# Performance work log

Measured on AMD Instinct MI355X. Metric: run time of the kernel, lower is better.

The kernel has to match this reference:

```python
import jax, jax.numpy as jnp
import numpy as np

TOP_K = 2  # config.moe_config.top_k


def setup_inputs() -> dict:
    key = jax.random.key(0)
    k0, k1, k2, k3 = jax.random.split(key, 4)
    T, H, I, E = 8192, 2048, 1408, 8  # tokens, hidden, moe_intermediate, experts
    x = jax.random.normal(k0, (T, H), jnp.float32)
    router_weight = jax.random.normal(k1, (E, H), jnp.float32) * 0.02
    gate_up_proj = jax.random.normal(k2, (E, H, 2 * I), jnp.float32) * 0.02
    down_proj = jax.random.normal(k3, (E, I, H), jnp.float32) * 0.02
    return {"x": x, "router_weight": router_weight,
            "gate_up_proj": gate_up_proj, "down_proj": down_proj}


def _moe_forward(x, router_weight, gate_up_proj, down_proj):
    # Router: fp32 gating linear (no bias), softmax over experts, top-k,
    # then scatter the top-k softmax weights into a dense [T, E] gate tensor
    # (topk_version=False path of Router.top_k_softmax).
    T = x.shape[0]
    E = router_weight.shape[0]
    logits = x.astype(jnp.float32) @ router_weight.T            # [T, E]
    probs = jax.nn.softmax(logits, axis=-1)                      # [T, E]
    topk_w, topk_idx = jax.lax.top_k(probs, TOP_K)               # [T, k]
    gates = jnp.zeros_like(logits).at[
        jnp.arange(T)[:, None], topk_idx].set(topk_w)            # [T, E] sparse gates

    # Grouped expert MLP (GroupedMLP): merged gate/up GEMM, SwiGLU, down GEMM.
    # Dispatch/permute + grouped GEMM + weighted combine is mathematically
    # out[t] = sum_e gates[t, e] * MLP_e(x[t]); expressed here as a fixed loop
    # over the small expert set with masked accumulation (jit-friendly).
    out = jnp.zeros_like(x)
    for e in range(E):
        gu = x @ gate_up_proj[e]                                 # [T, 2I]
        g, u = jnp.split(gu, 2, axis=-1)
        h = (jax.nn.silu(g) * u) @ down_proj[e]                  # [T, H]
        out = out + gates[:, e:e + 1].astype(x.dtype) * h
    return out


def reference(x, router_weight, gate_up_proj, down_proj):
    return _moe_forward(x, router_weight, gate_up_proj, down_proj)
```

## Files before the change

### kernel.cpp

```cpp
#include <hip/hip_runtime.h>
#include <hip/hip_bf16.h>
#include <cstdint>
#include <cstddef>

#define T_TOK 8192
#define H_DIM 2048
#define I_DIM 1408
#define E_NUM 8
#define BM 128
#define BK 64
#define ROWS_CAP (2 * T_TOK + E_NUM * BM)
#define MAX_MT (ROWS_CAP / BM)
#define NT1 (I_DIM / 64)
#define NT2 (H_DIM / 128)

typedef __attribute__((ext_vector_type(8))) short short8;
typedef __attribute__((ext_vector_type(4))) float f32x4;
typedef __attribute__((ext_vector_type(8))) unsigned short bf16x8;
typedef __attribute__((ext_vector_type(4))) unsigned short bf16x4;
typedef __attribute__((ext_vector_type(8))) _Float16 h16x8;

static __device__ __forceinline__ unsigned short f2bf(float f) {
  unsigned u = __float_as_uint(f);
  u += 0x7FFFu + ((u >> 16) & 1u);
  return (unsigned short)(u >> 16);
}

static __device__ __forceinline__ void gld_lds16(const void* g, void* l) {
  __builtin_amdgcn_global_load_lds(
      (__attribute__((address_space(1))) unsigned int*)g,
      (__attribute__((address_space(3))) unsigned int*)l, 16, 0, 0);
}

static __device__ __forceinline__ void remap_tile(int bid, int nb, int nt_cols,
                                                  int& m_t, int& n_t) {
  int chunk = nb >> 3;
  int wg = (bid & 7) * chunk + (bid >> 3);
  int grp = wg / (nt_cols * 4);
  int rem = wg % (nt_cols * 4);
  n_t = rem >> 2;
  m_t = grp * 4 + (rem & 3);
}

__global__ __launch_bounds__(256) void router_kernel(
    const float* __restrict__ x, const float* __restrict__ rw,
    int* __restrict__ topk_idx, float* __restrict__ topk_w, int* __restrict__ meta) {
  int t = blockIdx.x * 4 + (threadIdx.x >> 6);
  int lane = threadIdx.x & 63;
  const float* xr = x + (size_t)t * H_DIM;
  float acc[E_NUM];
#pragma unroll
  for (int e = 0; e < E_NUM; e++) acc[e] = 0.f;
  for (int j = lane; j < H_DIM; j += 64) {
    float xv = xr[j];
#pragma unroll
    for (int e = 0; e < E_NUM; e++) acc[e] += xv * rw[e * H_DIM + j];
  }
#pragma unroll
  for (int e = 0; e < E_NUM; e++) {
    float v = acc[e];
#pragma unroll
    for (int s = 32; s > 0; s >>= 1) v += __shfl_xor(v, s);
    acc[e] = v;
  }
  if (lane == 0) {
    int i0 = 0;
#pragma unroll
    for (int e = 1; e < E_NUM; e++) if (acc[e] > acc[i0]) i0 = e;
    int i1 = (i0 == 0) ? 1 : 0;
#pragma unroll
    for (int e = 0; e < E_NUM; e++) if (e != i0 && acc[e] > acc[i1]) i1 = e;
    float mx = acc[0];
#pragma unroll
    for (int e = 1; e < E_NUM; e++) mx = fmaxf(mx, acc[e]);
    float sum = 0.f, p[E_NUM];
#pragma unroll
    for (int e = 0; e < E_NUM; e++) { p[e] = expf(acc[e] - mx); sum += p[e]; }
    float inv = 1.f / sum;
    topk_idx[t * 2] = i0;  topk_idx[t * 2 + 1] = i1;
    topk_w[t * 2] = p[i0] * inv;  topk_w[t * 2 + 1] = p[i1] * inv;
    atomicAdd(&meta[i0], 1);
    atomicAdd(&meta[i1], 1);
  }
}

__global__ void scan_kernel(int* __restrict__ meta, int* __restrict__ row_token) {
  __shared__ int s_off[E_NUM + 1];
  if (threadIdx.x == 0) {
    int o = 0, nt = 0;
    for (int e = 0; e < E_NUM; e++) {
      meta[16 + e] = o; s_off[e] = o;
      int c = meta[e];
      int mtc = (c + BM - 1) / BM;
      for (int m = 0; m < mtc; m++) { meta[64 + nt] = e; meta[256 + nt] = o + m * BM; nt++; }
      o += mtc * BM;
      meta[8 + e] = 0;
    }
    meta[16 + E_NUM] = o; s_off[E_NUM] = o;
    meta[32] = nt;
  }
  __syncthreads();
  for (int e = 0; e < E_NUM; e++) {
    int lo = s_off[e] + meta[e], hi = s_off[e + 1];
    for (int r = lo + (int)threadIdx.x; r < hi; r += 64) row_token[r] = -1;
  }
}

__global__ __launch_bounds__(256) void bucket_kernel(
    const int* __restrict__ topk_idx, int* __restrict__ meta,
    int* __restrict__ row_token, int* __restrict__ tok2row) {
  int i = blockIdx.x * 256 + threadIdx.x;
  if (i >= 2 * T_TOK) return;
  int e = topk_idx[i];
  int pos = atomicAdd(&meta[8 + e], 1);
  int r = meta[16 + e] + pos;
  row_token[r] = i >> 1;
  tok2row[i] = r;
}

__global__ __launch_bounds__(256) void cvt_kernel(const float* __restrict__ in,
                                                  unsigned short* __restrict__ out, int n) {
  int i = (blockIdx.x * 256 + threadIdx.x) * 8;
  if (i >= n) return;
  bf16x8 v;
#pragma unroll
  for (int j = 0; j < 8; j++) v[j] = f2bf(in[i + j]);
  *(bf16x8*)(out + i) = v;
}

__global__ __launch_bounds__(256) void tcvt_kernel(const float* __restrict__ in,
                                                   unsigned short* __restrict__ out,
                                                   int R, int C) {
  __shared__ unsigned short tile[64][66];
  size_t ebase = (size_t)blockIdx.z * (size_t)R * (size_t)C;
  const float* src = in + ebase;
  unsigned short* dst = out + ebase;
  int c0 = blockIdx.x * 64, r0 = blockIdx.y * 64;
  int tid = threadIdx.x;
  int q = tid & 15, s = tid >> 4;
#pragma unroll
  for (int it = 0; it < 4; it++) {
    int rr = it * 16 + s;
    f32x4 v = *(const f32x4*)(src + (size_t)(r0 + rr) * C + c0 + q * 4);
#pragma unroll
    for (int j = 0; j < 4; j++) tile[rr][q * 4 + j] = f2bf(v[j]);
  }
  __syncthreads();
#pragma unroll
  for (int it = 0; it < 4; it++) {
    int cc = it * 16 + s;
    bf16x4 v;
#pragma unroll
    for (int j = 0; j < 4; j++) v[j] = tile[q * 4 + j][cc];
    *(bf16x4*)(dst + (size_t)(c0 + cc) * R + r0 + q * 4) = v;
  }
}

__global__ __launch_bounds__(256) void gemm1_kernel(
    const unsigned short* __restrict__ xb,
    const unsigned short* __restrict__ wgu,
    unsigned short* __restrict__ hbuf,
    const int* __restrict__ row_token, const int* __restrict__ meta) {
  int m_t, n_t;
  remap_tile(blockIdx.x, NT1 * MAX_MT, NT1, m_t, n_t);
  if (m_t >= meta[32]) return;
  int e = meta[64 + m_t];
  int row0 = meta[256 + m_t];
  int n0h = n_t * 64;

  __shared__ alignas(16) char smem[65536];

  int tid = threadIdx.x, lane = tid & 63, wid = tid >> 6;
  const unsigned short* asrc[4];
  const unsigned short* bsrc[4];
  {
    const unsigned short* wb = wgu + (size_t)e * (2 * (size_t)I_DIM) * H_DIM;
#pragma unroll
    for (int i = 0; i < 4; i++) {
      int r = i * 32 + (tid >> 3);
      int ch = ((tid & 7) ^ (r & 7)) * 8;
      int tok = row_token[row0 + r];
      if (tok < 0) tok = 0;
      asrc[i] = xb + (size_t)tok * H_DIM + ch;
      int wr = (r < 64) ? (n0h + r) : (I_DIM + n0h + (r - 64));
      bsrc[i] = wb + (size_t)wr * H_DIM + ch;
    }
  }
  f32x4 acc[4][4] = {};
  int mrow = (wid >> 1) * 64 + (lane & 15);
  int brow = (wid & 1) * 64 + (lane & 15);

#define STAGE1(buf, kof_)                                                     \
  {                                                                           \
    int kof = (kof_);                                                         \
    char* b = smem + (buf) * 32768;                                           \
    _Pragma("unroll") for (int i = 0; i < 4; i++) {                           \
      gld_lds16(asrc[i] + kof, b + i * 4096 + wid * 1024);                    \
      gld_lds16(bsrc[i] + kof, b + 16384 + i * 4096 + wid * 1024);            \
    }                                                                         \
  }

  STAGE1(0, 0);
  __syncthreads();
  int cur = 0;
  for (int kt = 0; kt < H_DIM / BK; kt++) {
    if (kt + 1 < H_DIM / BK) STAGE1(cur ^ 1, (kt + 1) * BK);
    const unsigned short* sA = (const unsigned short*)(smem + cur * 32768);
    const unsigned short* sB = sA + 8192;
#pragma unroll
    for (int kk = 0; kk < 2; kk++) {
      int krd = ((kk * 4 + (lane >> 4)) ^ (lane & 7)) * 8;
      short8 af[4], bf[4];
#pragma unroll
      for (int f = 0; f < 4; f++) {
        af[f] = *(const short8*)(sA + (mrow + f * 16) * BK + krd);
        bf[f] = *(const short8*)(sB + (brow + f * 16) * BK + krd);
      }
#pragma unroll
      for (int fm = 0; fm < 4; fm++)
#pragma unroll
        for (int fn = 0; fn < 4; fn++)
          acc[fm][fn] = __builtin_amdgcn_mfma_f32_16x16x32_bf16(af[fm], bf[fn], acc[fm][fn], 0, 0, 0);
    }
    __syncthreads();
    cur ^= 1;
  }

  float* xw = (float*)smem + (wid >> 1) * 4096;
  if (wid & 1) {
#pragma unroll
    for (int fm = 0; fm < 4; fm++)
#pragma unroll
      for (int r = 0; r < 4; r++) {
        int mloc = fm * 16 + (lane >> 4) * 4 + r;
#pragma unroll
        for (int fn = 0; fn < 4; fn++)
          xw[mloc * 64 + fn * 16 + (lane & 15)] = acc[fm][fn][r];
      }
  }
  __syncthreads();
  if (!(wid & 1)) {
    int mbase = row0 + (wid >> 1) * 64;
#pragma unroll
    for (int fm = 0; fm < 4; fm++)
#pragma unroll
      for (int r = 0; r < 4; r++) {
        int mloc = fm * 16 + (lane >> 4) * 4 + r;
        size_t rbase = (size_t)(mbase + mloc) * I_DIM + n0h;
#pragma unroll
        for (int fn = 0; fn < 4; fn++) {
          float g = acc[fm][fn][r];
          float u = xw[mloc * 64 + fn * 16 + (lane & 15)];
          float hv = (g / (1.f + __expf(-g))) * u;
          hbuf[rbase + fn * 16 + (lane & 15)] = f2bf(hv);
        }
      }
  }
}

__global__ __launch_bounds__(256) void gemm2_kernel(
    const unsigned short* __restrict__ hbuf,
    const unsigned short* __restrict__ wd,
    _Float16* __restrict__ part,
    const int* __restrict__ meta) {
  int m_t, n_t;
  remap_tile(blockIdx.x, NT2 * MAX_MT, NT2, m_t, n_t);
  if (m_t >= meta[32]) return;
  int e = meta[64 + m_t];
  int row0 = meta[256 + m_t];
  int n0 = n_t * 128;

  __shared__ alignas(16) char smem[65536];

  int tid = threadIdx.x, lane = tid & 63, wid = tid >> 6;
  const unsigned short* asrc[4];
  const unsigned short* bsrc[4];
  {
    const unsigned short* wb = wd + (size_t)e * (size_t)H_DIM * I_DIM;
#pragma unroll
    for (int i = 0; i < 4; i++) {
      int r = i * 32 + (tid >> 3);
      int ch = ((tid & 7) ^ (r & 7)) * 8;
      asrc[i] = hbuf + (size_t)(row0 + r) * I_DIM + ch;
      bsrc[i] = wb + (size_t)(n0 + r) * I_DIM + ch;
    }
  }
  f32x4 acc[4][4] = {};
  int mrow = (wid >> 1) * 64 + (lane & 15);
  int brow = (wid & 1) * 64 + (lane & 15);

  STAGE1(0, 0);
  __syncthreads();
  int cur = 0;
  for (int kt = 0; kt < I_DIM / BK; kt++) {
    if (kt + 1 < I_DIM / BK) STAGE1(cur ^ 1, (kt + 1) * BK);
    const unsigned short* sA = (const unsigned short*)(smem + cur * 32768);
    const unsigned short* sB = sA + 8192;
#pragma unroll
    for (int kk = 0; kk < 2; kk++) {
      int krd = ((kk * 4 + (lane >> 4)) ^ (lane & 7)) * 8;
      short8 af[4], bf[4];
#pragma unroll
      for (int f = 0; f < 4; f++) {
        af[f] = *(const short8*)(sA + (mrow + f * 16) * BK + krd);
        bf[f] = *(const short8*)(sB + (brow + f * 16) * BK + krd);
      }
#pragma unroll
      for (int fm = 0; fm < 4; fm++)
#pragma unroll
        for (int fn = 0; fn < 4; fn++)
          acc[fm][fn] = __builtin_amdgcn_mfma_f32_16x16x32_bf16(af[fm], bf[fn], acc[fm][fn], 0, 0, 0);
    }
    __syncthreads();
    cur ^= 1;
  }
  int m0 = (wid >> 1) * 64;
  int nn0 = n0 + (wid & 1) * 64 + (lane & 15);
#pragma unroll
  for (int fm = 0; fm < 4; fm++)
#pragma unroll
    for (int r = 0; r < 4; r++) {
      int rr = row0 + m0 + fm * 16 + (lane >> 4) * 4 + r;
      _Float16* prow = part + (size_t)rr * H_DIM + nn0;
#pragma unroll
      for (int fn = 0; fn < 4; fn++)
        prow[fn * 16] = (_Float16)acc[fm][fn][r];
    }
}

__global__ __launch_bounds__(256) void combine_kernel(
    const _Float16* __restrict__ part, const int* __restrict__ tok2row,
    const float* __restrict__ topk_w, float* __restrict__ out) {
  int t = blockIdx.x;
  int c = threadIdx.x * 8;
  int r0 = tok2row[2 * t], r1 = tok2row[2 * t + 1];
  float w0 = topk_w[2 * t], w1 = topk_w[2 * t + 1];
  h16x8 p0 = *(const h16x8*)(part + (size_t)r0 * H_DIM + c);
  h16x8 p1 = *(const h16x8*)(part + (size_t)r1 * H_DIM + c);
  float* o = out + (size_t)t * H_DIM + c;
  f32x4 lo, hi;
#pragma unroll
  for (int j = 0; j < 4; j++) lo[j] = w0 * (float)p0[j] + w1 * (float)p1[j];
#pragma unroll
  for (int j = 0; j < 4; j++) hi[j] = w0 * (float)p0[4 + j] + w1 * (float)p1[4 + j];
  *(f32x4*)o = lo;
  *(f32x4*)(o + 4) = hi;
}

extern "C" void kernel_launch(void* const* d_in, const int* in_sizes, int n_in,
                              void* d_out, int out_size, void* d_ws, size_t ws_size,
                              hipStream_t stream) {
  const float* x   = (const float*)d_in[0];
  const float* rw  = (const float*)d_in[1];
  const float* wgu = (const float*)d_in[2];
  const float* wdn = (const float*)d_in[3];
  float* out = (float*)d_out;

  char* ws = (char*)d_ws;
  size_t off = 0;
  auto alloc = [&](size_t bytes) {
    void* p = ws + off;
    off += (bytes + 255) & ~(size_t)255;
    return p;
  };
  int* meta            = (int*)alloc(4096);
  int* topk_idx        = (int*)alloc((size_t)2 * T_TOK * 4);
  float* topk_w        = (float*)alloc((size_t)2 * T_TOK * 4);
  int* tok2row         = (int*)alloc((size_t)2 * T_TOK * 4);
  int* row_token       = (int*)alloc((size_t)ROWS_CAP * 4);
  unsigned short* xb    = (unsigned short*)alloc((size_t)T_TOK * H_DIM * 2);
  unsigned short* wgu_t = (unsigned short*)alloc((size_t)E_NUM * 2 * I_DIM * H_DIM * 2);
  unsigned short* wd_t  = (unsigned short*)alloc((size_t)E_NUM * H_DIM * I_DIM * 2);
  unsigned short* hbuf  = (unsigned short*)alloc((size_t)ROWS_CAP * I_DIM * 2);
  _Float16* part = (_Float16*)wgu_t;

  if (off > ws_size) {
    (void)hipMemsetAsync(d_out, 0, (size_t)out_size * sizeof(float), stream);
    return;
  }

  (void)hipMemsetAsync(meta, 0, 4096, stream);

  cvt_kernel<<<(T_TOK * H_DIM / 8 + 255) / 256, 256, 0, stream>>>(x, xb, T_TOK * H_DIM);
  tcvt_kernel<<<dim3(2 * I_DIM / 64, H_DIM / 64, E_NUM), 256, 0, stream>>>(wgu, wgu_t, H_DIM, 2 * I_DIM);
  tcvt_kernel<<<dim3(H_DIM / 64, I_DIM / 64, E_NUM), 256, 0, stream>>>(wdn, wd_t, I_DIM, H_DIM);

  router_kernel<<<T_TOK / 4, 256, 0, stream>>>(x, rw, topk_idx, topk_w, meta);
  scan_kernel<<<1, 64, 0, stream>>>(meta, row_token);
  bucket_kernel<<<(2 * T_TOK + 255) / 256, 256, 0, stream>>>(topk_idx, meta, row_token, tok2row);

  gemm1_kernel<<<NT1 * MAX_MT, 256, 0, stream>>>(xb, wgu_t, hbuf, row_token, meta);
  gemm2_kernel<<<NT2 * MAX_MT, 256, 0, stream>>>(hbuf, wd_t, part, meta);
  combine_kernel<<<T_TOK, 256, 0, stream>>>(part, tok2row, topk_w, out);
}
```

Baseline: 776.7 us.

## Fuse x bf16 conversion into router and vectorize stores via LDS staging

Folds the standalone x-to-bf16 conversion into the router kernel, which now reads x with 128-bit loads and writes the bf16 copy while computing logits. This removes one kernel launch and a second full read of x. The weight transpose-convert kernel transposes while writing into LDS so it can emit 16-byte global stores. The GEMM1 SwiGLU and GEMM2 fp16 epilogues now stage results in shared memory and write 16-byte coalesced rows instead of scattered 2-byte stores. The cost is extra LDS traffic, possible bank conflicts and register pressure in the epilogues.

```diff
diff --git a/kernel.cpp b/kernel.cpp
--- a/kernel.cpp
+++ b/kernel.cpp
@@ -44,17 +44,26 @@
 
 __global__ __launch_bounds__(256) void router_kernel(
     const float* __restrict__ x, const float* __restrict__ rw,
+    unsigned short* __restrict__ xb,
     int* __restrict__ topk_idx, float* __restrict__ topk_w, int* __restrict__ meta) {
   int t = blockIdx.x * 4 + (threadIdx.x >> 6);
   int lane = threadIdx.x & 63;
   const float* xr = x + (size_t)t * H_DIM;
+  unsigned short* xbr = xb + (size_t)t * H_DIM;
   float acc[E_NUM];
 #pragma unroll
   for (int e = 0; e < E_NUM; e++) acc[e] = 0.f;
-  for (int j = lane; j < H_DIM; j += 64) {
-    float xv = xr[j];
-#pragma unroll
-    for (int e = 0; e < E_NUM; e++) acc[e] += xv * rw[e * H_DIM + j];
+  for (int j = lane * 4; j < H_DIM; j += 256) {
+    f32x4 v = *(const f32x4*)(xr + j);
+    bf16x4 b;
+#pragma unroll
+    for (int u = 0; u < 4; u++) b[u] = f2bf(v[u]);
+    *(bf16x4*)(xbr + j) = b;
+#pragma unroll
+    for (int e = 0; e < E_NUM; e++) {
+      f32x4 w = *(const f32x4*)(rw + e * H_DIM + j);
+      acc[e] += v[0] * w[0] + v[1] * w[1] + v[2] * w[2] + v[3] * w[3];
+    }
   }
 #pragma unroll
   for (int e = 0; e < E_NUM; e++) {
@@ -118,20 +127,10 @@
   tok2row[i] = r;
 }
 
-__global__ __launch_bounds__(256) void cvt_kernel(const float* __restrict__ in,
-                                                  unsigned short* __restrict__ out, int n) {
-  int i = (blockIdx.x * 256 + threadIdx.x) * 8;
-  if (i >= n) return;
-  bf16x8 v;
-#pragma unroll
-  for (int j = 0; j < 8; j++) v[j] = f2bf(in[i + j]);
-  *(bf16x8*)(out + i) = v;
-}
-
 __global__ __launch_bounds__(256) void tcvt_kernel(const float* __restrict__ in,
                                                    unsigned short* __restrict__ out,
                                                    int R, int C) {
-  __shared__ unsigned short tile[64][66];
+  __shared__ unsigned short st[64][72];
   size_t ebase = (size_t)blockIdx.z * (size_t)R * (size_t)C;
   const float* src = in + ebase;
   unsigned short* dst = out + ebase;
@@ -143,16 +142,15 @@
     int rr = it * 16 + s;
     f32x4 v = *(const f32x4*)(src + (size_t)(r0 + rr) * C + c0 + q * 4);
 #pragma unroll
-    for (int j = 0; j < 4; j++) tile[rr][q * 4 + j] = f2bf(v[j]);
+    for (int j = 0; j < 4; j++) st[q * 4 + j][rr] = f2bf(v[j]);
   }
   __syncthreads();
-#pragma unroll
-  for (int it = 0; it < 4; it++) {
-    int cc = it * 16 + s;
-    bf16x4 v;
-#pragma unroll
-    for (int j = 0; j < 4; j++) v[j] = tile[q * 4 + j][cc];
-    *(bf16x4*)(dst + (size_t)(c0 + cc) * R + r0 + q * 4) = v;
+  int cc = tid >> 3, rseg = (tid & 7) * 8;
+#pragma unroll
+  for (int it = 0; it < 2; it++) {
+    int c = it * 32 + cc;
+    bf16x8 v = *(const bf16x8*)(&st[c][rseg]);
+    *(bf16x8*)(dst + (size_t)(c0 + c) * R + r0 + rseg) = v;
   }
 }
 
@@ -240,21 +238,38 @@
   }
   __syncthreads();
   if (!(wid & 1)) {
-    int mbase = row0 + (wid >> 1) * 64;
+    unsigned short hv64[4][4][4];
 #pragma unroll
     for (int fm = 0; fm < 4; fm++)
 #pragma unroll
       for (int r = 0; r < 4; r++) {
         int mloc = fm * 16 + (lane >> 4) * 4 + r;
-        size_t rbase = (size_t)(mbase + mloc) * I_DIM + n0h;
 #pragma unroll
         for (int fn = 0; fn < 4; fn++) {
           float g = acc[fm][fn][r];
           float u = xw[mloc * 64 + fn * 16 + (lane & 15)];
           float hv = (g / (1.f + __expf(-g))) * u;
-          hbuf[rbase + fn * 16 + (lane & 15)] = f2bf(hv);
+          hv64[fm][r][fn] = f2bf(hv);
         }
       }
+    unsigned short* stg = (unsigned short*)smem + (wid >> 1) * 8192;
+#pragma unroll
+    for (int fm = 0; fm < 4; fm++)
+#pragma unroll
+      for (int r = 0; r < 4; r++) {
+        int mloc = fm * 16 + (lane >> 4) * 4 + r;
+#pragma unroll
+        for (int fn = 0; fn < 4; fn++)
+          stg[mloc * 64 + fn * 16 + (lane & 15)] = hv64[fm][r][fn];
+      }
+    int mbase = row0 + (wid >> 1) * 64;
+#pragma unroll
+    for (int it = 0; it < 8; it++) {
+      int mloc = it * 8 + (lane >> 3);
+      int cseg = (lane & 7) * 8;
+      bf16x8 v = *(const bf16x8*)(stg + mloc * 64 + cseg);
+      *(bf16x8*)(hbuf + (size_t)(mbase + mloc) * I_DIM + n0h + cseg) = v;
+    }
   }
 }
 
@@ -314,18 +329,25 @@
     __syncthreads();
     cur ^= 1;
   }
+  _Float16* stg = (_Float16*)(smem + wid * 8192);
+#pragma unroll
+  for (int fm = 0; fm < 4; fm++)
+#pragma unroll
+    for (int r = 0; r < 4; r++) {
+      int mloc = fm * 16 + (lane >> 4) * 4 + r;
+#pragma unroll
+      for (int fn = 0; fn < 4; fn++)
+        stg[mloc * 64 + fn * 16 + (lane & 15)] = (_Float16)acc[fm][fn][r];
+    }
   int m0 = (wid >> 1) * 64;
-  int nn0 = n0 + (wid & 1) * 64 + (lane & 15);
-#pragma unroll
-  for (int fm = 0; fm < 4; fm++)
-#pragma unroll
-    for (int r = 0; r < 4; r++) {
-      int rr = row0 + m0 + fm * 16 + (lane >> 4) * 4 + r;
-      _Float16* prow = part + (size_t)rr * H_DIM + nn0;
-#pragma unroll
-      for (int fn = 0; fn < 4; fn++)
-        prow[fn * 16] = (_Float16)acc[fm][fn][r];
-    }
+  int nbase = n0 + (wid & 1) * 64;
+#pragma unroll
+  for (int it = 0; it < 8; it++) {
+    int mloc = it * 8 + (lane >> 3);
+    int cseg = (lane & 7) * 8;
+    h16x8 v = *(const h16x8*)(stg + mloc * 64 + cseg);
+    *(h16x8*)(part + (size_t)(row0 + m0 + mloc) * H_DIM + nbase + cseg) = v;
+  }
 }
 
 __global__ __launch_bounds__(256) void combine_kernel(
@@ -381,11 +403,10 @@
 
   (void)hipMemsetAsync(meta, 0, 4096, stream);
 
-  cvt_kernel<<<(T_TOK * H_DIM / 8 + 255) / 256, 256, 0, stream>>>(x, xb, T_TOK * H_DIM);
   tcvt_kernel<<<dim3(2 * I_DIM / 64, H_DIM / 64, E_NUM), 256, 0, stream>>>(wgu, wgu_t, H_DIM, 2 * I_DIM);
   tcvt_kernel<<<dim3(H_DIM / 64, I_DIM / 64, E_NUM), 256, 0, stream>>>(wdn, wd_t, I_DIM, H_DIM);
 
-  router_kernel<<<T_TOK / 4, 256, 0, stream>>>(x, rw, topk_idx, topk_w, meta);
+  router_kernel<<<T_TOK / 4, 256, 0, stream>>>(x, rw, xb, topk_idx, topk_w, meta);
   scan_kernel<<<1, 64, 0, stream>>>(meta, row_token);
   bucket_kernel<<<(2 * T_TOK + 255) / 256, 256, 0, stream>>>(topk_idx, meta, row_token, tok2row);
 
```

Measured after the change: 764.6 us. Within noise of the previous version (-1.6%).
